# Kernel optimization log

Hardware: AMD Instinct MI355X
Metric: run time of the kernel (lower is better)

## Reference

```python
import jax, jax.numpy as jnp
import numpy as np
from jax import lax

B, T, L = 32, 512, 128
E, D, A, V = 1024, 1024, 512, 5000
C, FILTS = 10, 100
K = 2 * FILTS + 1
SOS = V - 1
SCALING = 2.0  # AttLoc softmax sharpening factor


def setup_inputs() -> dict:
    key = jax.random.key(0)
    ks = jax.random.split(key, 16)
    s = 0.02
    n = lambda k, sh: jax.random.normal(k, sh, jnp.float32) * s
    return {
        "hs_pad": jax.random.normal(ks[0], (B, T, E), jnp.float32),
        "hlens": jax.random.randint(ks[1], (B,), T // 2, T + 1, jnp.int32),
        "ys_pad": jax.random.randint(ks[2], (B, L), 0, V - 1, jnp.int32),
        "embed_W": n(ks[3], (V, D)),
        "w_ih0": n(ks[4], (4 * D, D + E)), "w_hh0": n(ks[5], (4 * D, D)),
        "b_ih0": jnp.zeros((4 * D,), jnp.float32), "b_hh0": jnp.zeros((4 * D,), jnp.float32),
        "w_ih1": n(ks[6], (4 * D, D)), "w_hh1": n(ks[7], (4 * D, D)),
        "b_ih1": jnp.zeros((4 * D,), jnp.float32), "b_hh1": jnp.zeros((4 * D,), jnp.float32),
        "att_enc_W": n(ks[8], (A, E)), "att_enc_b": jnp.zeros((A,), jnp.float32),
        "att_dec_W": n(ks[9], (A, D)),
        "att_conv_W": n(ks[10], (C, 1, K)),
        "att_att_W": n(ks[11], (A, C)),
        "gvec_W": n(ks[12], (1, A)), "gvec_b": jnp.zeros((1,), jnp.float32),
        "out_W": n(ks[13], (V, D)), "out_b": jnp.zeros((V,), jnp.float32),
    }


def lstm_cell(x, h, c, w_ih, w_hh, b_ih, b_hh):
    gates = x @ w_ih.T + h @ w_hh.T + b_ih + b_hh
    i, f, g, o = jnp.split(gates, 4, axis=-1)
    c = jax.nn.sigmoid(f) * c + jax.nn.sigmoid(i) * jnp.tanh(g)
    h = jax.nn.sigmoid(o) * jnp.tanh(c)
    return h, c


def _forward(hs_pad, hlens, ys_pad, embed_W, w_ih0, w_hh0, b_ih0, b_hh0,
             w_ih1, w_hh1, b_ih1, b_hh1, att_enc_W, att_enc_b, att_dec_W,
             att_conv_W, att_att_W, gvec_W, gvec_b, out_W, out_b):
    mask = jnp.arange(T)[None, :] < hlens[:, None]          # [B,T]
    pre_enc = jnp.einsum('bte,ae->bta', hs_pad, att_enc_W) + att_enc_b  # [B,T,A]
    # ys_in = [sos] + y (no padding: all targets full length)
    ys_in = jnp.concatenate([jnp.full((B, 1), SOS, ys_pad.dtype), ys_pad], axis=1)  # [B,L+1]
    eys = embed_W[ys_in]                                    # [B,L+1,D]
    aw0 = mask.astype(jnp.float32) / hlens[:, None].astype(jnp.float32)  # uniform init att
    z = jnp.zeros((B, D), jnp.float32)

    def step(carry, ey_t):
        z0, c0, z1, c1, aw = carry
        # location-aware attention (AttLoc)
        conv = lax.conv_general_dilated(aw[:, None, :], att_conv_W, (1,),
                                        [(FILTS, FILTS)],
                                        dimension_numbers=('NCH', 'OIH', 'NCH'))  # [B,C,T]
        conv_proj = jnp.einsum('bct,ac->bta', conv, att_att_W)
        dec_proj = z0 @ att_dec_W.T                          # [B,A]
        e = jnp.tanh(pre_enc + conv_proj + dec_proj[:, None, :]) @ gvec_W[0] + gvec_b[0]  # [B,T]
        e = jnp.where(mask, e, -1e9)
        aw = jax.nn.softmax(SCALING * e, axis=1)
        att_c = jnp.einsum('bt,bte->be', aw, hs_pad)         # [B,E]
        ey = jnp.concatenate([ey_t, att_c], axis=-1)         # [B,D+E]
        z0, c0 = lstm_cell(ey, z0, c0, w_ih0, w_hh0, b_ih0, b_hh0)
        z1, c1 = lstm_cell(z0, z1, c1, w_ih1, w_hh1, b_ih1, b_hh1)
        return (z0, c0, z1, c1, aw), z1

    _, zs = lax.scan(step, (z, z, z, z, aw0), jnp.swapaxes(eys, 0, 1))  # zs: [L+1,B,D]
    y_all = jnp.einsum('lbd,vd->blv', zs, out_W) + out_b     # [B,L+1,V]
    return y_all


def reference(hs_pad, hlens, ys_pad, embed_W, w_ih0, w_hh0, b_ih0, b_hh0,
              w_ih1, w_hh1, b_ih1, b_hh1, att_enc_W, att_enc_b, att_dec_W,
              att_conv_W, att_att_W, gvec_W, gvec_b, out_W, out_b):
    return _forward(hs_pad, hlens, ys_pad, embed_W, w_ih0, w_hh0, b_ih0, b_hh0,
                    w_ih1, w_hh1, b_ih1, b_hh1, att_enc_W, att_enc_b, att_dec_W,
                    att_conv_W, att_att_W, gvec_W, gvec_b, out_W, out_b)
```

## Files before the change

### kernel.cpp

```cpp
#include <hip/hip_runtime.h>
#include <cstdint>
#include <cstddef>

#define BB 32
#define TT 512
#define NSTEPS 129
#define EE 1024
#define DD 1024
#define AAD 512
#define VV 5000
#define SOS 4999
#define KW 201
#define NFILT 100

__device__ __forceinline__ float fsig(float x){
    return __fdividef(1.0f, 1.0f + __expf(-x));
}
__device__ __forceinline__ float ftanh(float x){
    float ax = fabsf(x);
    float e = __expf(-2.0f*ax);
    float r = __fdividef(1.0f - e, 1.0f + e);
    return copysignf(r, x);
}

__global__ void k_init(const int* __restrict__ hlens, float* __restrict__ aw,
                       float* __restrict__ x0, float* __restrict__ x1,
                       float* __restrict__ g1, float* __restrict__ c0,
                       float* __restrict__ c1)
{
    int idx = blockIdx.x*256 + threadIdx.x;
    if (idx < BB*TT){
        int b = idx >> 9;
        int t = idx & 511;
        int hl = hlens[b];
        aw[idx] = (t < hl) ? __fdividef(1.0f, (float)hl) : 0.0f;
    }
    if (idx < BB*1024){
        int b = idx >> 10, d = idx & 1023;
        x0[b*3072 + 2048 + d] = 0.0f;
        x1[b*2048 + 1024 + d] = 0.0f;
        c0[idx] = 0.0f;
        c1[idx] = 0.0f;
    }
    if (idx < BB*AAD){
        int b = idx >> 9, a = idx & 511;
        g1[b*4608 + 4096 + a] = 0.0f;
    }
}

template<bool GUARD, bool REMAP>
__global__ __launch_bounds__(256) void k_gemm_nt(
    const float* __restrict__ Am, const float* __restrict__ Bm,
    const float* __restrict__ bias, float* __restrict__ Cm,
    int M, int N, int K)
{
    __shared__ float as[16][132];
    __shared__ float bs[16][68];
    const int tid = threadIdx.x;
    const int m0 = blockIdx.x * 128, n0 = blockIdx.y * 64;
    const int tm = tid & 15, tn = tid >> 4;
    float acc[8][4];
#pragma unroll
    for (int i = 0; i < 8; ++i)
#pragma unroll
        for (int j = 0; j < 4; ++j) acc[i][j] = 0.0f;

    for (int k0 = 0; k0 < K; k0 += 16){
#pragma unroll
        for (int i = 0; i < 2; ++i){
            int idx = tid + i*256;
            int r = idx >> 2, q = idx & 3;
            int row = m0 + r;
            float4 v = make_float4(0.f,0.f,0.f,0.f);
            if (!GUARD || row < M) v = *(const float4*)(Am + (size_t)row*K + k0 + q*4);
            as[q*4+0][r] = v.x; as[q*4+1][r] = v.y;
            as[q*4+2][r] = v.z; as[q*4+3][r] = v.w;
        }
        {
            int r = tid >> 2, q = tid & 3;
            int row = n0 + r;
            float4 v = make_float4(0.f,0.f,0.f,0.f);
            if (!GUARD || row < N) v = *(const float4*)(Bm + (size_t)row*K + k0 + q*4);
            bs[q*4+0][r] = v.x; bs[q*4+1][r] = v.y;
            bs[q*4+2][r] = v.z; bs[q*4+3][r] = v.w;
        }
        __syncthreads();
#pragma unroll
        for (int kk = 0; kk < 16; ++kk){
            float4 a0 = *(const float4*)&as[kk][tm*8];
            float4 a1 = *(const float4*)&as[kk][tm*8+4];
            float4 b0 = *(const float4*)&bs[kk][tn*4];
            float av[8] = {a0.x,a0.y,a0.z,a0.w,a1.x,a1.y,a1.z,a1.w};
            float bv[4] = {b0.x,b0.y,b0.z,b0.w};
#pragma unroll
            for (int i = 0; i < 8; ++i)
#pragma unroll
                for (int j = 0; j < 4; ++j) acc[i][j] += av[i]*bv[j];
        }
        __syncthreads();
    }
#pragma unroll
    for (int i = 0; i < 8; ++i){
        int m = m0 + tm*8 + i;
        if (GUARD && m >= M) continue;
#pragma unroll
        for (int j = 0; j < 4; ++j){
            int n = n0 + tn*4 + j;
            if (GUARD && n >= N) continue;
            float v = acc[i][j] + bias[n];
            size_t dst;
            if (REMAP){
                dst = ((size_t)(m & 31) * NSTEPS + (size_t)(m >> 5)) * VV + (size_t)n;
            } else {
                dst = (size_t)m * (size_t)N + (size_t)n;
            }
            Cm[dst] = v;
        }
    }
}

__global__ __launch_bounds__(256) void k_e(
    const float* __restrict__ pre_enc, const float* __restrict__ aw,
    const float* __restrict__ g1,
    const float* __restrict__ conv_w,
    const float* __restrict__ att_att_W,
    const float* __restrict__ gvec_W,
    const float* __restrict__ gvec_b,
    float* __restrict__ e_out)
{
    __shared__ float awin[264];
    __shared__ float convs[10][64];
    __shared__ float watt_s[512*12];
    const int tc = blockIdx.x, b = blockIdx.y;
    const int t0 = tc * 64;
    const int tid = threadIdx.x;

    for (int idx = tid; idx < 264; idx += 256){
        int t = t0 - NFILT + idx;
        awin[idx] = (t >= 0 && t < TT) ? aw[b*TT + t] : 0.0f;
    }
    for (int idx = tid; idx < 5120; idx += 256){
        int a = idx / 10, c = idx % 10;
        watt_s[a*12 + c] = att_att_W[idx];
    }
    for (int idx = tid; idx < 512; idx += 256){
        watt_s[idx*12 + 10] = g1[b*4608 + 4096 + idx];
        watt_s[idx*12 + 11] = gvec_W[idx];
    }
    __syncthreads();

    for (int idx = tid; idx < 640; idx += 256){
        int c = idx >> 6, tl = idx & 63;
        const float* wc = conv_w + c*KW;
        float s = 0.0f;
#pragma unroll 4
        for (int k = 0; k < KW; ++k) s += awin[tl + k] * wc[k];
        convs[c][tl] = s;
    }
    __syncthreads();

    const int q = tid & 3, tl = tid >> 2;
    const int t = t0 + tl;
    float cv[10];
#pragma unroll
    for (int c = 0; c < 10; ++c) cv[c] = convs[c][tl];
    const float* pre_row = pre_enc + (size_t)(b*TT + t)*AAD;
    float acc = 0.0f;
#pragma unroll 4
    for (int j = 0; j < 128; ++j){
        int a = (j << 2) | q;
        const float* wr = &watt_s[a*12];
        float4 w0 = *(const float4*)wr;
        float4 w1 = *(const float4*)(wr+4);
        float4 w2 = *(const float4*)(wr+8);
        float cp = cv[0]*w0.x + cv[1]*w0.y + cv[2]*w0.z + cv[3]*w0.w
                 + cv[4]*w1.x + cv[5]*w1.y + cv[6]*w1.z + cv[7]*w1.w
                 + cv[8]*w2.x + cv[9]*w2.y;
        float v = pre_row[a] + w2.z + cp;
        acc += ftanh(v) * w2.w;
    }
    acc += __shfl_xor(acc, 1);
    acc += __shfl_xor(acc, 2);
    if (q == 0) e_out[b*TT + t] = acc + gvec_b[0];
}

__global__ __launch_bounds__(256) void k_soft_attc(
    const float* __restrict__ e_in, const float* __restrict__ hs,
    const int* __restrict__ hlens, const int* __restrict__ ys_pad,
    const float* __restrict__ embed_W,
    float* __restrict__ aw, float* __restrict__ x0, int s)
{
    __shared__ float p_s[512];
    __shared__ float red[256];
    const int qc = blockIdx.x, b = blockIdx.y;
    const int tid = threadIdx.x;
    const int hl = hlens[b];

    float e0 = e_in[b*TT + tid];
    float e1 = e_in[b*TT + 256 + tid];
    float v0 = 2.0f * e0;
    float v1 = (256 + tid < hl) ? 2.0f*e1 : -1e30f;
    float m = fmaxf(v0, v1);
#pragma unroll
    for (int ofs = 1; ofs < 64; ofs <<= 1) m = fmaxf(m, __shfl_xor(m, ofs));
    if ((tid & 63) == 0) red[tid >> 6] = m;
    __syncthreads();
    m = fmaxf(fmaxf(red[0], red[1]), fmaxf(red[2], red[3]));
    __syncthreads();

    float p0 = __expf(v0 - m);
    float p1 = (256 + tid < hl) ? __expf(v1 - m) : 0.0f;
    float sum = p0 + p1;
#pragma unroll
    for (int ofs = 1; ofs < 64; ofs <<= 1) sum += __shfl_xor(sum, ofs);
    if ((tid & 63) == 0) red[tid >> 6] = sum;
    __syncthreads();
    sum = red[0] + red[1] + red[2] + red[3];
    float rinv = 1.0f / sum;
    p_s[tid] = p0 * rinv;
    p_s[tid + 256] = p1 * rinv;
    if (qc == 0){
        aw[b*TT + tid] = p0 * rinv;
        aw[b*TT + 256 + tid] = p1 * rinv;
    }
    __syncthreads();

    const int i = tid & 127, th = tid >> 7;
    const int ec = qc*128 + i;
    const float* hrow = hs + (size_t)(b*TT + th*256)*EE + ec;
    float acc = 0.0f;
#pragma unroll 8
    for (int t = 0; t < 256; ++t) acc += p_s[th*256 + t] * hrow[(size_t)t*EE];
    red[tid] = acc;
    __syncthreads();
    if (th == 0){
        float attc = red[i] + red[128 + i];
        x0[b*3072 + 1024 + ec] = attc;
        int tok = (s == 0) ? SOS : ys_pad[b*128 + (s-1)];
        x0[b*3072 + qc*128 + tid] = embed_W[(size_t)tok*DD + qc*128 + tid];
    }
}

__global__ __launch_bounds__(256) void k_gates0(
    const float* __restrict__ x0, const float* __restrict__ w_ih0,
    const float* __restrict__ w_hh0, float* __restrict__ g0)
{
    const int tid = threadIdx.x;
    const int lane = tid & 63;
    const int b0 = (tid >> 6) * 8;
    const int n0 = blockIdx.x * 8;
    float acc[8][8];
#pragma unroll
    for (int i = 0; i < 8; ++i)
#pragma unroll
        for (int j = 0; j < 8; ++j) acc[i][j] = 0.0f;

    const float* xbase = x0 + (size_t)b0*3072;
    {
        const float* wbase = w_ih0 + (size_t)n0*2048;
        for (int kc = 0; kc < 8; ++kc){
            int kb = kc*256 + lane*4;
            float4 xv[8], wv[8];
#pragma unroll
            for (int i = 0; i < 8; ++i) xv[i] = *(const float4*)&xbase[i*3072 + kb];
#pragma unroll
            for (int j = 0; j < 8; ++j) wv[j] = *(const float4*)&wbase[j*2048 + kb];
#pragma unroll
            for (int i = 0; i < 8; ++i)
#pragma unroll
                for (int j = 0; j < 8; ++j)
                    acc[i][j] += xv[i].x*wv[j].x + xv[i].y*wv[j].y
                               + xv[i].z*wv[j].z + xv[i].w*wv[j].w;
        }
    }
    {
        const float* wbase = w_hh0 + (size_t)n0*1024;
        for (int kc = 0; kc < 4; ++kc){
            int kb = kc*256 + lane*4;
            float4 xv[8], wv[8];
#pragma unroll
            for (int i = 0; i < 8; ++i) xv[i] = *(const float4*)&xbase[i*3072 + 2048 + kb];
#pragma unroll
            for (int j = 0; j < 8; ++j) wv[j] = *(const float4*)&wbase[j*1024 + kb];
#pragma unroll
            for (int i = 0; i < 8; ++i)
#pragma unroll
                for (int j = 0; j < 8; ++j)
                    acc[i][j] += xv[i].x*wv[j].x + xv[i].y*wv[j].y
                               + xv[i].z*wv[j].z + xv[i].w*wv[j].w;
        }
    }
    float cur[64];
#pragma unroll
    for (int i = 0; i < 8; ++i)
#pragma unroll
        for (int j = 0; j < 8; ++j) cur[i*8+j] = acc[i][j];
#pragma unroll
    for (int rb = 0; rb < 6; ++rb){
        const int bit = 1 << rb;
        const int half = 32 >> rb;
        const bool up = (lane & bit) != 0;
#pragma unroll
        for (int i = 0; i < half; ++i){
            float lo = cur[i], hi = cur[i + half];
            float send = up ? lo : hi;
            float keep = up ? hi : lo;
            cur[i] = keep + __shfl_xor(send, bit);
        }
    }
    int ci = (int)(__brev((unsigned)lane) >> 26);
    int ib = ci >> 3, jn = ci & 7;
    g0[(b0 + ib)*4096 + n0 + jn] = cur[0];
}

__global__ __launch_bounds__(256) void k_gates1(
    const float* __restrict__ x1, const float* __restrict__ w_ih1,
    const float* __restrict__ w_hh1, const float* __restrict__ dec_W,
    float* __restrict__ g1)
{
    const int tid = threadIdx.x;
    const int lane = tid & 63;
    const int b0 = (tid >> 6) * 8;
    const int n0 = blockIdx.x * 8;
    const bool isdec = (n0 >= 4096);
    float acc[8][8];
#pragma unroll
    for (int i = 0; i < 8; ++i)
#pragma unroll
        for (int j = 0; j < 8; ++j) acc[i][j] = 0.0f;

    const float* xbase = x1 + (size_t)b0*2048;
    {
        const float* wbase = isdec ? dec_W + (size_t)(n0-4096)*1024
                                   : w_ih1 + (size_t)n0*1024;
        for (int kc = 0; kc < 4; ++kc){
            int kb = kc*256 + lane*4;
            float4 xv[8], wv[8];
#pragma unroll
            for (int i = 0; i < 8; ++i) xv[i] = *(const float4*)&xbase[i*2048 + kb];
#pragma unroll
            for (int j = 0; j < 8; ++j) wv[j] = *(const float4*)&wbase[j*1024 + kb];
#pragma unroll
            for (int i = 0; i < 8; ++i)
#pragma unroll
                for (int j = 0; j < 8; ++j)
                    acc[i][j] += xv[i].x*wv[j].x + xv[i].y*wv[j].y
                               + xv[i].z*wv[j].z + xv[i].w*wv[j].w;
        }
    }
    if (!isdec){
        const float* wbase = w_hh1 + (size_t)n0*1024;
        for (int kc = 0; kc < 4; ++kc){
            int kb = kc*256 + lane*4;
            float4 xv[8], wv[8];
#pragma unroll
            for (int i = 0; i < 8; ++i) xv[i] = *(const float4*)&xbase[i*2048 + 1024 + kb];
#pragma unroll
            for (int j = 0; j < 8; ++j) wv[j] = *(const float4*)&wbase[j*1024 + kb];
#pragma unroll
            for (int i = 0; i < 8; ++i)
#pragma unroll
                for (int j = 0; j < 8; ++j)
                    acc[i][j] += xv[i].x*wv[j].x + xv[i].y*wv[j].y
                               + xv[i].z*wv[j].z + xv[i].w*wv[j].w;
        }
    }
    float cur[64];
#pragma unroll
    for (int i = 0; i < 8; ++i)
#pragma unroll
        for (int j = 0; j < 8; ++j) cur[i*8+j] = acc[i][j];
#pragma unroll
    for (int rb = 0; rb < 6; ++rb){
        const int bit = 1 << rb;
        const int half = 32 >> rb;
        const bool up = (lane & bit) != 0;
#pragma unroll
        for (int i = 0; i < half; ++i){
            float lo = cur[i], hi = cur[i + half];
            float send = up ? lo : hi;
            float keep = up ? hi : lo;
            cur[i] = keep + __shfl_xor(send, bit);
        }
    }
    int ci = (int)(__brev((unsigned)lane) >> 26);
    int ib = ci >> 3, jn = ci & 7;
    g1[(b0 + ib)*4608 + n0 + jn] = cur[0];
}

__global__ void k_lstm0(const float* __restrict__ g0, const float* __restrict__ bi,
                        const float* __restrict__ bh, float* __restrict__ c0,
                        float* __restrict__ x0, float* __restrict__ x1)
{
    int idx = blockIdx.x*256 + threadIdx.x;
    int b = idx >> 10, d = idx & 1023;
    const float* gr = g0 + b*4096;
    float gi = gr[d]        + bi[d]        + bh[d];
    float gf = gr[1024 + d] + bi[1024 + d] + bh[1024 + d];
    float gg = gr[2048 + d] + bi[2048 + d] + bh[2048 + d];
    float go = gr[3072 + d] + bi[3072 + d] + bh[3072 + d];
    float c = fsig(gf)*c0[idx] + fsig(gi)*ftanh(gg);
    float h = fsig(go)*ftanh(c);
    c0[idx] = c;
    x0[b*3072 + 2048 + d] = h;
    x1[b*2048 + d] = h;
}

__global__ void k_lstm1(const float* __restrict__ g1, const float* __restrict__ bi,
                        const float* __restrict__ bh, float* __restrict__ c1,
                        float* __restrict__ x1, float* __restrict__ zs, int s)
{
    int idx = blockIdx.x*256 + threadIdx.x;
    int b = idx >> 10, d = idx & 1023;
    const float* gr = g1 + b*4608;
    float gi = gr[d]        + bi[d]        + bh[d];
    float gf = gr[1024 + d] + bi[1024 + d] + bh[1024 + d];
    float gg = gr[2048 + d] + bi[2048 + d] + bh[2048 + d];
    float go = gr[3072 + d] + bi[3072 + d] + bh[3072 + d];
    float c = fsig(gf)*c1[idx] + fsig(gi)*ftanh(gg);
    float h = fsig(go)*ftanh(c);
    c1[idx] = c;
    x1[b*2048 + 1024 + d] = h;
    zs[(size_t)(s*32 + b)*1024 + d] = h;
}

extern "C" void kernel_launch(void* const* d_in, const int* in_sizes, int n_in,
                              void* d_out, int out_size, void* d_ws, size_t ws_size,
                              hipStream_t stream)
{
    const float* hs      = (const float*)d_in[0];
    const int*   hlens   = (const int*)d_in[1];
    const int*   ys_pad  = (const int*)d_in[2];
    const float* embed_W = (const float*)d_in[3];
    const float* w_ih0   = (const float*)d_in[4];
    const float* w_hh0   = (const float*)d_in[5];
    const float* b_ih0   = (const float*)d_in[6];
    const float* b_hh0   = (const float*)d_in[7];
    const float* w_ih1   = (const float*)d_in[8];
    const float* w_hh1   = (const float*)d_in[9];
    const float* b_ih1   = (const float*)d_in[10];
    const float* b_hh1   = (const float*)d_in[11];
    const float* enc_W   = (const float*)d_in[12];
    const float* enc_b   = (const float*)d_in[13];
    const float* dec_W   = (const float*)d_in[14];
    const float* conv_W  = (const float*)d_in[15];
    const float* att_W   = (const float*)d_in[16];
    const float* gvec_W  = (const float*)d_in[17];
    const float* gvec_b  = (const float*)d_in[18];
    const float* out_W   = (const float*)d_in[19];
    const float* out_b   = (const float*)d_in[20];
    float* out = (float*)d_out;

    float* ws      = (float*)d_ws;
    float* pre_enc = ws;
    float* aw      = pre_enc + 8388608;
    float* e_buf   = aw + 16384;
    float* x0      = e_buf + 16384;
    float* x1      = x0 + 98304;
    float* g0      = x1 + 65536;
    float* g1      = g0 + 131072;
    float* c0      = g1 + 147456;
    float* c1      = c0 + 32768;
    float* zs      = c1 + 32768;

    k_init<<<128, 256, 0, stream>>>(hlens, aw, x0, x1, g1, c0, c1);
    k_gemm_nt<false,false><<<dim3(128, 8), 256, 0, stream>>>(
        hs, enc_W, enc_b, pre_enc, 16384, 512, 1024);

    for (int s = 0; s < NSTEPS; ++s){
        k_e<<<dim3(8, 32), 256, 0, stream>>>(pre_enc, aw, g1, conv_W, att_W,
                                             gvec_W, gvec_b, e_buf);
        k_soft_attc<<<dim3(8, 32), 256, 0, stream>>>(e_buf, hs, hlens, ys_pad,
                                                     embed_W, aw, x0, s);
        k_gates0<<<512, 256, 0, stream>>>(x0, w_ih0, w_hh0, g0);
        k_lstm0<<<128, 256, 0, stream>>>(g0, b_ih0, b_hh0, c0, x0, x1);
        k_gates1<<<576, 256, 0, stream>>>(x1, w_ih1, w_hh1, dec_W, g1);
        k_lstm1<<<128, 256, 0, stream>>>(g1, b_ih1, b_hh1, c1, x1, zs, s);
    }

    k_gemm_nt<true,true><<<dim3(33, 79), 256, 0, stream>>>(
        zs, out_W, out_b, out, 4128, 5000, 1024);
}
```

Before: 15.65 ms.

## Fuse decoder time loop into one persistent kernel with grid barriers

Replaces the six per-step kernel launches (774 launches total) with a single persistent kernel of 256 blocks that runs all 129 decoder steps, separated by a custom atomic grid barrier. Each block owns 4 hidden units across all four LSTM gates, so the gate GEMV and the cell update fuse, and the g0/g1 scratch round trips go away. Hidden states are double-buffered, and the decoder projection is computed alongside the layer-1 gates. This removes launch overhead and inter-kernel gaps, but adds four grid-wide barriers per step, lowers parallelism per phase, and relies on all 256 blocks being co-resident to avoid deadlock.

```diff
diff --git a/kernel.cpp b/kernel.cpp
--- a/kernel.cpp
+++ b/kernel.cpp
@@ -12,6 +12,8 @@
 #define SOS 4999
 #define KW 201
 #define NFILT 100
+#define NBLK 256
+#define NTHR 512
 
 __device__ __forceinline__ float fsig(float x){
     return __fdividef(1.0f, 1.0f + __expf(-x));
@@ -23,29 +25,66 @@
     return copysignf(r, x);
 }
 
+__device__ __forceinline__ void butterfly64(float* cur, int lane){
+#pragma unroll
+    for (int rb = 0; rb < 6; ++rb){
+        const int bit = 1 << rb;
+        const int half = 32 >> rb;
+        const bool up = (lane & bit) != 0;
+#pragma unroll
+        for (int i = 0; i < half; ++i){
+            float lo = cur[i], hi = cur[i + half];
+            float send = up ? lo : hi;
+            float keep = up ? hi : lo;
+            cur[i] = keep + __shfl_xor(send, bit);
+        }
+    }
+}
+
+__device__ __forceinline__ void gbar(int* flags, int* gen, int ep){
+    __syncthreads();
+    if (threadIdx.x == 0){
+        __threadfence();
+        __hip_atomic_store(&flags[blockIdx.x*16], ep, __ATOMIC_RELEASE,
+                           __HIP_MEMORY_SCOPE_AGENT);
+    }
+    if (blockIdx.x == 0){
+        if (threadIdx.x < NBLK){
+            while (__hip_atomic_load(&flags[threadIdx.x*16], __ATOMIC_RELAXED,
+                                     __HIP_MEMORY_SCOPE_AGENT) < ep)
+                __builtin_amdgcn_s_sleep(2);
+        }
+        __syncthreads();
+        if (threadIdx.x == 0)
+            __hip_atomic_store(gen, ep, __ATOMIC_RELEASE,
+                               __HIP_MEMORY_SCOPE_AGENT);
+    } else {
+        if (threadIdx.x == 0){
+            while (__hip_atomic_load(gen, __ATOMIC_RELAXED,
+                                     __HIP_MEMORY_SCOPE_AGENT) < ep)
+                __builtin_amdgcn_s_sleep(2);
+        }
+    }
+    if (threadIdx.x == 0) __threadfence();
+    __syncthreads();
+}
+
 __global__ void k_init(const int* __restrict__ hlens, float* __restrict__ aw,
-                       float* __restrict__ x0, float* __restrict__ x1,
-                       float* __restrict__ g1, float* __restrict__ c0,
-                       float* __restrict__ c1)
+                       float* __restrict__ z0a, float* __restrict__ z1a,
+                       float* __restrict__ g1dec, float* __restrict__ c0,
+                       float* __restrict__ c1, int* __restrict__ bar)
 {
     int idx = blockIdx.x*256 + threadIdx.x;
     if (idx < BB*TT){
-        int b = idx >> 9;
-        int t = idx & 511;
+        int b = idx >> 9, t = idx & 511;
         int hl = hlens[b];
         aw[idx] = (t < hl) ? __fdividef(1.0f, (float)hl) : 0.0f;
     }
     if (idx < BB*1024){
-        int b = idx >> 10, d = idx & 1023;
-        x0[b*3072 + 2048 + d] = 0.0f;
-        x1[b*2048 + 1024 + d] = 0.0f;
-        c0[idx] = 0.0f;
-        c1[idx] = 0.0f;
-    }
-    if (idx < BB*AAD){
-        int b = idx >> 9, a = idx & 511;
-        g1[b*4608 + 4096 + a] = 0.0f;
-    }
+        z0a[idx] = 0.0f; z1a[idx] = 0.0f; c0[idx] = 0.0f; c1[idx] = 0.0f;
+    }
+    if (idx < BB*AAD) g1dec[idx] = 0.0f;
+    if (idx < 8192)   bar[idx] = 0;
 }
 
 template<bool GUARD, bool REMAP>
@@ -119,309 +158,282 @@
     }
 }
 
-__global__ __launch_bounds__(256) void k_e(
-    const float* __restrict__ pre_enc, const float* __restrict__ aw,
-    const float* __restrict__ g1,
-    const float* __restrict__ conv_w,
-    const float* __restrict__ att_att_W,
-    const float* __restrict__ gvec_W,
+template<int XSA, int NCA, int LDA, int XSB, int NCB, int LDB>
+__device__ __forceinline__ void gates_16rows(
+    const float* __restrict__ xa, const float* __restrict__ wa,
+    const float* __restrict__ xb, const float* __restrict__ wb,
+    int d0, int b0, int lane, float* cur)
+{
+#pragma unroll
+    for (int k = 0; k < 64; ++k) cur[k] = 0.0f;
+    size_t ra[16], rb[16];
+#pragma unroll
+    for (int idx = 0; idx < 16; ++idx){
+        int r = (idx>>2)*1024 + d0 + (idx&3);
+        ra[idx] = (size_t)r * LDA;
+        rb[idx] = (size_t)r * LDB;
+    }
+    for (int kc = 0; kc < NCA; ++kc){
+        int kb = kc*256 + lane*4;
+        float4 xv[4];
+#pragma unroll
+        for (int i = 0; i < 4; ++i)
+            xv[i] = *(const float4*)&xa[(size_t)(b0+i)*XSA + kb];
+#pragma unroll
+        for (int g2 = 0; g2 < 2; ++g2){
+            float4 wv[8];
+#pragma unroll
+            for (int jj = 0; jj < 8; ++jj)
+                wv[jj] = *(const float4*)&wa[ra[g2*8+jj] + kb];
+#pragma unroll
+            for (int i = 0; i < 4; ++i)
+#pragma unroll
+                for (int jj = 0; jj < 8; ++jj)
+                    cur[i*16+g2*8+jj] += xv[i].x*wv[jj].x + xv[i].y*wv[jj].y
+                                       + xv[i].z*wv[jj].z + xv[i].w*wv[jj].w;
+        }
+    }
+    for (int kc = 0; kc < NCB; ++kc){
+        int kb = kc*256 + lane*4;
+        float4 xv[4];
+#pragma unroll
+        for (int i = 0; i < 4; ++i)
+            xv[i] = *(const float4*)&xb[(size_t)(b0+i)*XSB + kb];
+#pragma unroll
+        for (int g2 = 0; g2 < 2; ++g2){
+            float4 wv[8];
+#pragma unroll
+            for (int jj = 0; jj < 8; ++jj)
+                wv[jj] = *(const float4*)&wb[rb[g2*8+jj] + kb];
+#pragma unroll
+            for (int i = 0; i < 4; ++i)
+#pragma unroll
+                for (int jj = 0; jj < 8; ++jj)
+                    cur[i*16+g2*8+jj] += xv[i].x*wv[jj].x + xv[i].y*wv[jj].y
+                                       + xv[i].z*wv[jj].z + xv[i].w*wv[jj].w;
+        }
+    }
+}
+
+__global__ __launch_bounds__(NTHR, 2) void k_persist(
+    const float* __restrict__ hs, const int* __restrict__ hlens,
+    const int* __restrict__ ys_pad, const float* __restrict__ embed_W,
+    const float* __restrict__ w_ih0, const float* __restrict__ w_hh0,
+    const float* __restrict__ b_ih0, const float* __restrict__ b_hh0,
+    const float* __restrict__ w_ih1, const float* __restrict__ w_hh1,
+    const float* __restrict__ b_ih1, const float* __restrict__ b_hh1,
+    const float* __restrict__ dec_W, const float* __restrict__ conv_W,
+    const float* __restrict__ att_W, const float* __restrict__ gvec_W,
     const float* __restrict__ gvec_b,
-    float* __restrict__ e_out)
+    const float* __restrict__ pre_enc, float* __restrict__ aw,
+    float* __restrict__ e_buf, float* __restrict__ x0,
+    float* __restrict__ z0a, float* __restrict__ z0b,
+    float* __restrict__ z1a, float* __restrict__ z1b,
+    float* __restrict__ g1dec, float* __restrict__ c0,
+    float* __restrict__ c1, float* __restrict__ zs, int* __restrict__ bar)
 {
-    __shared__ float awin[264];
-    __shared__ float convs[10][64];
-    __shared__ float watt_s[512*12];
-    const int tc = blockIdx.x, b = blockIdx.y;
+    __shared__ float watt[AAD*12];
+    __shared__ float cws[2016];
+    __shared__ float aws[264];
+    __shared__ float convs[640];
+    __shared__ float ps[512];
+    __shared__ float red[512];
+    __shared__ float gs[32][17];
+    __shared__ float decpart[512];
+    __shared__ float bsum0[16], bsum1[16];
+
+    const int blk  = blockIdx.x;
+    const int tid  = threadIdx.x;
+    const int w    = tid >> 6;
+    const int lane = tid & 63;
+    int* flags = bar;
+    int* gen   = bar + 4096;
+
+    const int b1 = blk >> 3;
+    const int tc = blk & 7;
     const int t0 = tc * 64;
-    const int tid = threadIdx.x;
-
-    for (int idx = tid; idx < 264; idx += 256){
-        int t = t0 - NFILT + idx;
-        awin[idx] = (t >= 0 && t < TT) ? aw[b*TT + t] : 0.0f;
-    }
-    for (int idx = tid; idx < 5120; idx += 256){
-        int a = idx / 10, c = idx % 10;
-        watt_s[a*12 + c] = att_att_W[idx];
-    }
-    for (int idx = tid; idx < 512; idx += 256){
-        watt_s[idx*12 + 10] = g1[b*4608 + 4096 + idx];
-        watt_s[idx*12 + 11] = gvec_W[idx];
+    const int ch = blk & 7;
+    const int d0 = blk * 4;
+    const int rd0 = blk * 2;
+    const int hl = hlens[b1];
+    const float gb0 = gvec_b[0];
+
+    for (int idx = tid; idx < AAD*10; idx += NTHR)
+        watt[(idx/10)*12 + (idx%10)] = att_W[idx];
+    for (int idx = tid; idx < AAD; idx += NTHR)
+        watt[idx*12 + 11] = gvec_W[idx];
+    for (int idx = tid; idx < 10*KW; idx += NTHR)
+        cws[idx] = conv_W[idx];
+    if (tid < 16){
+        int r = (tid>>2)*1024 + d0 + (tid&3);
+        bsum0[tid] = b_ih0[r] + b_hh0[r];
+        bsum1[tid] = b_ih1[r] + b_hh1[r];
     }
     __syncthreads();
 
-    for (int idx = tid; idx < 640; idx += 256){
-        int c = idx >> 6, tl = idx & 63;
-        const float* wc = conv_w + c*KW;
-        float s = 0.0f;
+    int ep = 0;
+    for (int s = 0; s < NSTEPS; ++s){
+        float* z0in  = (s & 1) ? z0b : z0a;
+        float* z0out = (s & 1) ? z0a : z0b;
+        float* z1in  = (s & 1) ? z1b : z1a;
+        float* z1out = (s & 1) ? z1a : z1b;
+
+        {
+            watt[tid*12 + 10] = g1dec[b1*AAD + tid];
+            if (tid < 264){
+                int t = t0 - NFILT + tid;
+                aws[tid] = (t >= 0 && t < TT) ? aw[b1*TT + t] : 0.0f;
+            }
+            __syncthreads();
+            for (int idx = tid; idx < 640; idx += NTHR){
+                int c = idx >> 6, tl = idx & 63;
+                const float* wc = &cws[c*KW];
+                float sacc = 0.0f;
 #pragma unroll 4
-        for (int k = 0; k < KW; ++k) s += awin[tl + k] * wc[k];
-        convs[c][tl] = s;
-    }
-    __syncthreads();
-
-    const int q = tid & 3, tl = tid >> 2;
-    const int t = t0 + tl;
-    float cv[10];
-#pragma unroll
-    for (int c = 0; c < 10; ++c) cv[c] = convs[c][tl];
-    const float* pre_row = pre_enc + (size_t)(b*TT + t)*AAD;
-    float acc = 0.0f;
+                for (int k = 0; k < KW; ++k) sacc += aws[tl + k] * wc[k];
+                convs[c*64 + tl] = sacc;
+            }
+            __syncthreads();
+            const int q = tid & 7, tl = tid >> 3;
+            const int t = t0 + tl;
+            float cv[10];
+#pragma unroll
+            for (int c = 0; c < 10; ++c) cv[c] = convs[c*64 + tl];
+            const float* pre_row = pre_enc + (size_t)(b1*TT + t)*AAD;
+            float acc = 0.0f;
 #pragma unroll 4
-    for (int j = 0; j < 128; ++j){
-        int a = (j << 2) | q;
-        const float* wr = &watt_s[a*12];
-        float4 w0 = *(const float4*)wr;
-        float4 w1 = *(const float4*)(wr+4);
-        float4 w2 = *(const float4*)(wr+8);
-        float cp = cv[0]*w0.x + cv[1]*w0.y + cv[2]*w0.z + cv[3]*w0.w
-                 + cv[4]*w1.x + cv[5]*w1.y + cv[6]*w1.z + cv[7]*w1.w
-                 + cv[8]*w2.x + cv[9]*w2.y;
-        float v = pre_row[a] + w2.z + cp;
-        acc += ftanh(v) * w2.w;
-    }
-    acc += __shfl_xor(acc, 1);
-    acc += __shfl_xor(acc, 2);
-    if (q == 0) e_out[b*TT + t] = acc + gvec_b[0];
-}
-
-__global__ __launch_bounds__(256) void k_soft_attc(
-    const float* __restrict__ e_in, const float* __restrict__ hs,
-    const int* __restrict__ hlens, const int* __restrict__ ys_pad,
-    const float* __restrict__ embed_W,
-    float* __restrict__ aw, float* __restrict__ x0, int s)
-{
-    __shared__ float p_s[512];
-    __shared__ float red[256];
-    const int qc = blockIdx.x, b = blockIdx.y;
-    const int tid = threadIdx.x;
-    const int hl = hlens[b];
-
-    float e0 = e_in[b*TT + tid];
-    float e1 = e_in[b*TT + 256 + tid];
-    float v0 = 2.0f * e0;
-    float v1 = (256 + tid < hl) ? 2.0f*e1 : -1e30f;
-    float m = fmaxf(v0, v1);
-#pragma unroll
-    for (int ofs = 1; ofs < 64; ofs <<= 1) m = fmaxf(m, __shfl_xor(m, ofs));
-    if ((tid & 63) == 0) red[tid >> 6] = m;
-    __syncthreads();
-    m = fmaxf(fmaxf(red[0], red[1]), fmaxf(red[2], red[3]));
-    __syncthreads();
-
-    float p0 = __expf(v0 - m);
-    float p1 = (256 + tid < hl) ? __expf(v1 - m) : 0.0f;
-    float sum = p0 + p1;
-#pragma unroll
-    for (int ofs = 1; ofs < 64; ofs <<= 1) sum += __shfl_xor(sum, ofs);
-    if ((tid & 63) == 0) red[tid >> 6] = sum;
-    __syncthreads();
-    sum = red[0] + red[1] + red[2] + red[3];
-    float rinv = 1.0f / sum;
-    p_s[tid] = p0 * rinv;
-    p_s[tid + 256] = p1 * rinv;
-    if (qc == 0){
-        aw[b*TT + tid] = p0 * rinv;
-        aw[b*TT + 256 + tid] = p1 * rinv;
-    }
-    __syncthreads();
-
-    const int i = tid & 127, th = tid >> 7;
-    const int ec = qc*128 + i;
-    const float* hrow = hs + (size_t)(b*TT + th*256)*EE + ec;
-    float acc = 0.0f;
+            for (int j = 0; j < 64; ++j){
+                int a = (j << 3) | q;
+                const float* wr = &watt[a*12];
+                float4 w0 = *(const float4*)wr;
+                float4 w1 = *(const float4*)(wr+4);
+                float4 w2 = *(const float4*)(wr+8);
+                float cp = cv[0]*w0.x + cv[1]*w0.y + cv[2]*w0.z + cv[3]*w0.w
+                         + cv[4]*w1.x + cv[5]*w1.y + cv[6]*w1.z + cv[7]*w1.w
+                         + cv[8]*w2.x + cv[9]*w2.y;
+                float v = pre_row[a] + w2.z + cp;
+                acc += ftanh(v) * w2.w;
+            }
+            acc += __shfl_xor(acc, 1);
+            acc += __shfl_xor(acc, 2);
+            acc += __shfl_xor(acc, 4);
+            if (q == 0) e_buf[b1*TT + t] = acc + gb0;
+        }
+        ep++; gbar(flags, gen, ep);
+
+        {
+            float ev = e_buf[b1*TT + tid];
+            float v = (tid < hl) ? 2.0f*ev : -1e30f;
+            float m = v;
+#pragma unroll
+            for (int ofs = 1; ofs < 64; ofs <<= 1) m = fmaxf(m, __shfl_xor(m, ofs));
+            if (lane == 0) red[w] = m;
+            __syncthreads();
+            m = red[0];
+#pragma unroll
+            for (int k = 1; k < 8; ++k) m = fmaxf(m, red[k]);
+            __syncthreads();
+            float p = __expf(v - m);
+            float su = p;
+#pragma unroll
+            for (int ofs = 1; ofs < 64; ofs <<= 1) su += __shfl_xor(su, ofs);
+            if (lane == 0) red[w] = su;
+            __syncthreads();
+            su = red[0];
+#pragma unroll
+            for (int k = 1; k < 8; ++k) su += red[k];
+            float rinv = 1.0f / su;
+            float pn = p * rinv;
+            ps[tid] = pn;
+            if (ch == 0) aw[b1*TT + tid] = pn;
+            __syncthreads();
+            const int c = tid & 127, th = tid >> 7;
+            const int col = ch*128 + c;
+            const float* hcol = hs + (size_t)(b1*TT + th*128)*EE + col;
+            float acc = 0.0f;
 #pragma unroll 8
-    for (int t = 0; t < 256; ++t) acc += p_s[th*256 + t] * hrow[(size_t)t*EE];
-    red[tid] = acc;
-    __syncthreads();
-    if (th == 0){
-        float attc = red[i] + red[128 + i];
-        x0[b*3072 + 1024 + ec] = attc;
-        int tok = (s == 0) ? SOS : ys_pad[b*128 + (s-1)];
-        x0[b*3072 + qc*128 + tid] = embed_W[(size_t)tok*DD + qc*128 + tid];
-    }
-}
-
-__global__ __launch_bounds__(256) void k_gates0(
-    const float* __restrict__ x0, const float* __restrict__ w_ih0,
-    const float* __restrict__ w_hh0, float* __restrict__ g0)
-{
-    const int tid = threadIdx.x;
-    const int lane = tid & 63;
-    const int b0 = (tid >> 6) * 8;
-    const int n0 = blockIdx.x * 8;
-    float acc[8][8];
-#pragma unroll
-    for (int i = 0; i < 8; ++i)
-#pragma unroll
-        for (int j = 0; j < 8; ++j) acc[i][j] = 0.0f;
-
-    const float* xbase = x0 + (size_t)b0*3072;
-    {
-        const float* wbase = w_ih0 + (size_t)n0*2048;
-        for (int kc = 0; kc < 8; ++kc){
-            int kb = kc*256 + lane*4;
-            float4 xv[8], wv[8];
-#pragma unroll
-            for (int i = 0; i < 8; ++i) xv[i] = *(const float4*)&xbase[i*3072 + kb];
-#pragma unroll
-            for (int j = 0; j < 8; ++j) wv[j] = *(const float4*)&wbase[j*2048 + kb];
-#pragma unroll
-            for (int i = 0; i < 8; ++i)
-#pragma unroll
-                for (int j = 0; j < 8; ++j)
-                    acc[i][j] += xv[i].x*wv[j].x + xv[i].y*wv[j].y
-                               + xv[i].z*wv[j].z + xv[i].w*wv[j].w;
-        }
-    }
-    {
-        const float* wbase = w_hh0 + (size_t)n0*1024;
-        for (int kc = 0; kc < 4; ++kc){
-            int kb = kc*256 + lane*4;
-            float4 xv[8], wv[8];
-#pragma unroll
-            for (int i = 0; i < 8; ++i) xv[i] = *(const float4*)&xbase[i*3072 + 2048 + kb];
-#pragma unroll
-            for (int j = 0; j < 8; ++j) wv[j] = *(const float4*)&wbase[j*1024 + kb];
-#pragma unroll
-            for (int i = 0; i < 8; ++i)
-#pragma unroll
-                for (int j = 0; j < 8; ++j)
-                    acc[i][j] += xv[i].x*wv[j].x + xv[i].y*wv[j].y
-                               + xv[i].z*wv[j].z + xv[i].w*wv[j].w;
-        }
-    }
-    float cur[64];
-#pragma unroll
-    for (int i = 0; i < 8; ++i)
-#pragma unroll
-        for (int j = 0; j < 8; ++j) cur[i*8+j] = acc[i][j];
-#pragma unroll
-    for (int rb = 0; rb < 6; ++rb){
-        const int bit = 1 << rb;
-        const int half = 32 >> rb;
-        const bool up = (lane & bit) != 0;
-#pragma unroll
-        for (int i = 0; i < half; ++i){
-            float lo = cur[i], hi = cur[i + half];
-            float send = up ? lo : hi;
-            float keep = up ? hi : lo;
-            cur[i] = keep + __shfl_xor(send, bit);
-        }
-    }
-    int ci = (int)(__brev((unsigned)lane) >> 26);
-    int ib = ci >> 3, jn = ci & 7;
-    g0[(b0 + ib)*4096 + n0 + jn] = cur[0];
-}
-
-__global__ __launch_bounds__(256) void k_gates1(
-    const float* __restrict__ x1, const float* __restrict__ w_ih1,
-    const float* __restrict__ w_hh1, const float* __restrict__ dec_W,
-    float* __restrict__ g1)
-{
-    const int tid = threadIdx.x;
-    const int lane = tid & 63;
-    const int b0 = (tid >> 6) * 8;
-    const int n0 = blockIdx.x * 8;
-    const bool isdec = (n0 >= 4096);
-    float acc[8][8];
-#pragma unroll
-    for (int i = 0; i < 8; ++i)
-#pragma unroll
-        for (int j = 0; j < 8; ++j) acc[i][j] = 0.0f;
-
-    const float* xbase = x1 + (size_t)b0*2048;
-    {
-        const float* wbase = isdec ? dec_W + (size_t)(n0-4096)*1024
-                                   : w_ih1 + (size_t)n0*1024;
-        for (int kc = 0; kc < 4; ++kc){
-            int kb = kc*256 + lane*4;
-            float4 xv[8], wv[8];
-#pragma unroll
-            for (int i = 0; i < 8; ++i) xv[i] = *(const float4*)&xbase[i*2048 + kb];
-#pragma unroll
-            for (int j = 0; j < 8; ++j) wv[j] = *(const float4*)&wbase[j*1024 + kb];
-#pragma unroll
-            for (int i = 0; i < 8; ++i)
-#pragma unroll
-                for (int j = 0; j < 8; ++j)
-                    acc[i][j] += xv[i].x*wv[j].x + xv[i].y*wv[j].y
-                               + xv[i].z*wv[j].z + xv[i].w*wv[j].w;
-        }
-    }
-    if (!isdec){
-        const float* wbase = w_hh1 + (size_t)n0*1024;
-        for (int kc = 0; kc < 4; ++kc){
-            int kb = kc*256 + lane*4;
-            float4 xv[8], wv[8];
-#pragma unroll
-            for (int i = 0; i < 8; ++i) xv[i] = *(const float4*)&xbase[i*2048 + 1024 + kb];
-#pragma unroll
-            for (int j = 0; j < 8; ++j) wv[j] = *(const float4*)&wbase[j*1024 + kb];
-#pragma unroll
-            for (int i = 0; i < 8; ++i)
-#pragma unroll
-                for (int j = 0; j < 8; ++j)
-                    acc[i][j] += xv[i].x*wv[j].x + xv[i].y*wv[j].y
-                               + xv[i].z*wv[j].z + xv[i].w*wv[j].w;
-        }
-    }
-    float cur[64];
-#pragma unroll
-    for (int i = 0; i < 8; ++i)
-#pragma unroll
-        for (int j = 0; j < 8; ++j) cur[i*8+j] = acc[i][j];
-#pragma unroll
-    for (int rb = 0; rb < 6; ++rb){
-        const int bit = 1 << rb;
-        const int half = 32 >> rb;
-        const bool up = (lane & bit) != 0;
-#pragma unroll
-        for (int i = 0; i < half; ++i){
-            float lo = cur[i], hi = cur[i + half];
-            float send = up ? lo : hi;
-            float keep = up ? hi : lo;
-            cur[i] = keep + __shfl_xor(send, bit);
-        }
-    }
-    int ci = (int)(__brev((unsigned)lane) >> 26);
-    int ib = ci >> 3, jn = ci & 7;
-    g1[(b0 + ib)*4608 + n0 + jn] = cur[0];
-}
-
-__global__ void k_lstm0(const float* __restrict__ g0, const float* __restrict__ bi,
-                        const float* __restrict__ bh, float* __restrict__ c0,
-                        float* __restrict__ x0, float* __restrict__ x1)
-{
-    int idx = blockIdx.x*256 + threadIdx.x;
-    int b = idx >> 10, d = idx & 1023;
-    const float* gr = g0 + b*4096;
-    float gi = gr[d]        + bi[d]        + bh[d];
-    float gf = gr[1024 + d] + bi[1024 + d] + bh[1024 + d];
-    float gg = gr[2048 + d] + bi[2048 + d] + bh[2048 + d];
-    float go = gr[3072 + d] + bi[3072 + d] + bh[3072 + d];
-    float c = fsig(gf)*c0[idx] + fsig(gi)*ftanh(gg);
-    float h = fsig(go)*ftanh(c);
-    c0[idx] = c;
-    x0[b*3072 + 2048 + d] = h;
-    x1[b*2048 + d] = h;
-}
-
-__global__ void k_lstm1(const float* __restrict__ g1, const float* __restrict__ bi,
-                        const float* __restrict__ bh, float* __restrict__ c1,
-                        float* __restrict__ x1, float* __restrict__ zs, int s)
-{
-    int idx = blockIdx.x*256 + threadIdx.x;
-    int b = idx >> 10, d = idx & 1023;
-    const float* gr = g1 + b*4608;
-    float gi = gr[d]        + bi[d]        + bh[d];
-    float gf = gr[1024 + d] + bi[1024 + d] + bh[1024 + d];
-    float gg = gr[2048 + d] + bi[2048 + d] + bh[2048 + d];
-    float go = gr[3072 + d] + bi[3072 + d] + bh[3072 + d];
-    float c = fsig(gf)*c1[idx] + fsig(gi)*ftanh(gg);
-    float h = fsig(go)*ftanh(c);
-    c1[idx] = c;
-    x1[b*2048 + 1024 + d] = h;
-    zs[(size_t)(s*32 + b)*1024 + d] = h;
+            for (int t2 = 0; t2 < 128; ++t2)
+                acc += ps[th*128 + t2] * hcol[(size_t)t2*EE];
+            red[tid] = acc;
+            __syncthreads();
+            if (th == 0){
+                float attc = red[c] + red[c+128] + red[c+256] + red[c+384];
+                x0[b1*2048 + 1024 + col] = attc;
+                int tok = (s == 0) ? SOS : ys_pad[b1*128 + (s-1)];
+                x0[b1*2048 + ch*128 + c] = embed_W[(size_t)tok*DD + ch*128 + c];
+            }
+        }
+        ep++; gbar(flags, gen, ep);
+
+        {
+            const int b0 = w * 4;
+            float cur[64];
+            gates_16rows<2048,8,2048, 1024,4,1024>(x0, w_ih0, z0in, w_hh0,
+                                                   d0, b0, lane, cur);
+            butterfly64(cur, lane);
+            int ci = (int)(__brev((unsigned)lane) >> 26);
+            gs[b0 + (ci>>4)][ci & 15] = cur[0];
+            __syncthreads();
+            if (tid < 128){
+                int b = tid >> 2, dl = tid & 3, d = d0 + dl;
+                float gi = gs[b][dl]      + bsum0[dl];
+                float gf = gs[b][4 + dl]  + bsum0[4 + dl];
+                float gg = gs[b][8 + dl]  + bsum0[8 + dl];
+                float go = gs[b][12 + dl] + bsum0[12 + dl];
+                float c = fsig(gf)*c0[b*1024 + d] + fsig(gi)*ftanh(gg);
+                float h = fsig(go)*ftanh(c);
+                c0[b*1024 + d] = c;
+                z0out[b*1024 + d] = h;
+            }
+        }
+        ep++; gbar(flags, gen, ep);
+
+        {
+            const int b0 = w * 4;
+            float cur[64];
+            gates_16rows<1024,4,1024, 1024,4,1024>(z0out, w_ih1, z1in, w_hh1,
+                                                   d0, b0, lane, cur);
+            butterfly64(cur, lane);
+            int ci = (int)(__brev((unsigned)lane) >> 26);
+            gs[b0 + (ci>>4)][ci & 15] = cur[0];
+            {
+                int ks = w*128 + lane*2;
+                float2 dv0 = *(const float2*)&dec_W[(size_t)rd0*1024 + ks];
+                float2 dv1 = *(const float2*)&dec_W[(size_t)(rd0+1)*1024 + ks];
+                float cd[64];
+#pragma unroll
+                for (int b = 0; b < 32; ++b){
+                    float2 zv = *(const float2*)&z0out[b*1024 + ks];
+                    cd[b*2]   = zv.x*dv0.x + zv.y*dv0.y;
+                    cd[b*2+1] = zv.x*dv1.x + zv.y*dv1.y;
+                }
+                butterfly64(cd, lane);
+                int ci2 = (int)(__brev((unsigned)lane) >> 26);
+                decpart[w*64 + ci2] = cd[0];
+            }
+            __syncthreads();
+            if (tid < 128){
+                int b = tid >> 2, dl = tid & 3, d = d0 + dl;
+                float gi = gs[b][dl]      + bsum1[dl];
+                float gf = gs[b][4 + dl]  + bsum1[4 + dl];
+                float gg = gs[b][8 + dl]  + bsum1[8 + dl];
+                float go = gs[b][12 + dl] + bsum1[12 + dl];
+                float c = fsig(gf)*c1[b*1024 + d] + fsig(gi)*ftanh(gg);
+                float h = fsig(go)*ftanh(c);
+                c1[b*1024 + d] = c;
+                z1out[b*1024 + d] = h;
+                zs[(size_t)(s*32 + b)*1024 + d] = h;
+            } else if (tid < 192){
+                int o = tid - 128;
+                float v = 0.0f;
+#pragma unroll
+                for (int wv = 0; wv < 8; ++wv) v += decpart[wv*64 + o];
+                int b = o >> 1, rl = o & 1;
+                g1dec[b*AAD + rd0 + rl] = v;
+            }
+        }
+        ep++; gbar(flags, gen, ep);
+    }
 }
 
 extern "C" void kernel_launch(void* const* d_in, const int* in_sizes, int n_in,
@@ -456,27 +468,27 @@
     float* aw      = pre_enc + 8388608;
     float* e_buf   = aw + 16384;
     float* x0      = e_buf + 16384;
-    float* x1      = x0 + 98304;
-    float* g0      = x1 + 65536;
-    float* g1      = g0 + 131072;
-    float* c0      = g1 + 147456;
+    float* z0a     = x0 + 65536;
+    float* z0b     = z0a + 32768;
+    float* z1a     = z0b + 32768;
+    float* z1b     = z1a + 32768;
+    float* g1dec   = z1b + 32768;
+    float* c0      = g1dec + 16384;
     float* c1      = c0 + 32768;
     float* zs      = c1 + 32768;
-
-    k_init<<<128, 256, 0, stream>>>(hlens, aw, x0, x1, g1, c0, c1);
+    int*   bar     = (int*)(zs + 4227072);
+
+    k_init<<<128, 256, 0, stream>>>(hlens, aw, z0a, z1a, g1dec, c0, c1, bar);
     k_gemm_nt<false,false><<<dim3(128, 8), 256, 0, stream>>>(
         hs, enc_W, enc_b, pre_enc, 16384, 512, 1024);
 
-    for (int s = 0; s < NSTEPS; ++s){
-        k_e<<<dim3(8, 32), 256, 0, stream>>>(pre_enc, aw, g1, conv_W, att_W,
-                                             gvec_W, gvec_b, e_buf);
-        k_soft_attc<<<dim3(8, 32), 256, 0, stream>>>(e_buf, hs, hlens, ys_pad,
-                                                     embed_W, aw, x0, s);
-        k_gates0<<<512, 256, 0, stream>>>(x0, w_ih0, w_hh0, g0);
-        k_lstm0<<<128, 256, 0, stream>>>(g0, b_ih0, b_hh0, c0, x0, x1);
-        k_gates1<<<576, 256, 0, stream>>>(x1, w_ih1, w_hh1, dec_W, g1);
-        k_lstm1<<<128, 256, 0, stream>>>(g1, b_ih1, b_hh1, c1, x1, zs, s);
-    }
+    k_persist<<<NBLK, NTHR, 0, stream>>>(
+        hs, hlens, ys_pad, embed_W,
+        w_ih0, w_hh0, b_ih0, b_hh0,
+        w_ih1, w_hh1, b_ih1, b_hh1,
+        dec_W, conv_W, att_W, gvec_W, gvec_b,
+        pre_enc, aw, e_buf, x0, z0a, z0b, z1a, z1b,
+        g1dec, c0, c1, zs, bar);
 
     k_gemm_nt<true,true><<<dim3(33, 79), 256, 0, stream>>>(
         zs, out_W, out_b, out, 4128, 5000, 1024);
```

Measured after the change: 22.00 ms. +40.6%, slower.
